# Optimization experiments

Measured on AMD Instinct MI355X. Metric: run time of the kernel, lower is better.

The kernel has to match this reference:

```python
import jax, jax.numpy as jnp
import numpy as np

B, T, C = 4, 2048, 2048
H, S = 32, 64
LN_EPS = 1e-5


def _layer_norm(x, w, b):
    mu = jnp.mean(x, axis=-1, keepdims=True)
    var = jnp.mean((x - mu) ** 2, axis=-1, keepdims=True)
    return (x - mu) / jnp.sqrt(var + LN_EPS) * w + b


def setup_inputs() -> dict:
    key = jax.random.key(0)
    ks = jax.random.split(key, 8)
    sc = 1.0 / np.sqrt(C)
    sc4 = 1.0 / np.sqrt(4 * C)
    return {
        "x": jax.random.normal(ks[0], (B, T, C), jnp.float32),
        "time_decay": jnp.full((H, S), -5.0, jnp.float32),
        "time_first": jnp.zeros((H, S), jnp.float32),
        "Wk": jax.random.normal(ks[1], (C, C), jnp.float32) * sc,
        "Wv": jax.random.normal(ks[2], (C, C), jnp.float32) * sc,
        "Wr": jax.random.normal(ks[3], (C, C), jnp.float32) * sc,
        "Wo": jax.random.normal(ks[4], (C, C), jnp.float32) * sc,
        "Wfk": jax.random.normal(ks[5], (C, 4 * C), jnp.float32) * sc,
        "Wfv": jax.random.normal(ks[6], (4 * C, C), jnp.float32) * sc4,
        "ln1_w": jnp.ones((C,), jnp.float32),
        "ln1_b": jnp.zeros((C,), jnp.float32),
        "ln2_w": jnp.ones((C,), jnp.float32),
        "ln2_b": jnp.zeros((C,), jnp.float32),
    }


def reference(x, time_decay, time_first, Wk, Wv, Wr, Wo, Wfk, Wfv,
              ln1_w, ln1_b, ln2_w, ln2_b):
    b, t, c = x.shape
    h, s = time_decay.shape
    xl = _layer_norm(x, ln1_w, ln1_b)
    k = (xl @ Wk).reshape(b, t, h, s)  # [B,T,H,S]
    v = (xl @ Wv).reshape(b, t, h, s)
    r = (xl @ Wr).reshape(b, t, h, s)

    decay = jnp.exp(-jnp.exp(time_decay))  # [H,S]
    u = jnp.exp(k) * v                      # [B,T,H,S]
    u_t = jnp.swapaxes(u, 0, 1)             # [T,B,H,S]

    def step(state, ut):
        state = decay * state + ut
        return state, state

    _, states = jax.lax.scan(step, jnp.zeros((b, h, s), x.dtype), u_t)  # [T,B,H,S]
    # t=0 bonus term: exp(time_first) * v_0 added to wkv only (not the state)
    states = states.at[0].add(jnp.exp(time_first) * v[:, 0])
    wkv = jnp.swapaxes(states, 0, 1)        # [B,T,H,S]

    rwkv = jax.nn.sigmoid(r) * wkv
    x = x + rwkv.reshape(b, t, c) @ Wo
    xl2 = _layer_norm(x, ln2_w, ln2_b)
    ffn = (jax.nn.relu(xl2 @ Wfk) ** 2) @ Wfv
    return x + ffn
```

## Files before the change

kernel.cpp:

```cpp
#include <hip/hip_runtime.h>
#include <hip/hip_bf16.h>
#include <stdint.h>

#define B_  4
#define T_  2048
#define C_  2048
#define H_  32
#define S_  64
#define M_  (B_ * T_)
#define C4_ (4 * C_)
#define C2_ (2 * C_)
#define LN_EPS 1e-5f
#define NCH 16
#define CLEN 128
#define NCHAN (B_ * C_)

typedef unsigned short u16;
typedef __attribute__((ext_vector_type(8))) short short8;
typedef __attribute__((ext_vector_type(4))) float f32x4;

__device__ __forceinline__ u16 f2bf(float f) {
  uint32_t u = __float_as_uint(f);
  u = (u + 0x7FFFu + ((u >> 16) & 1u)) >> 16;
  return (u16)u;
}
__device__ __forceinline__ float bf2f(u16 u) {
  return __uint_as_float(((uint32_t)u) << 16);
}

__device__ __forceinline__ void gload_lds16(const void* g, void* l) {
  __builtin_amdgcn_global_load_lds(
      (const __attribute__((address_space(1))) uint32_t*)g,
      (__attribute__((address_space(3))) uint32_t*)l, 16, 0, 0);
}

__global__ __launch_bounds__(256) void k_transpose_cast(
    const float* __restrict__ in, u16* __restrict__ out, int ld, int R, int Cn) {
  __shared__ float tile[32][33];
  const int tx = threadIdx.x & 31, ty = threadIdx.x >> 5;
  const int c0 = blockIdx.x * 32, r0 = blockIdx.y * 32;
#pragma unroll
  for (int i = 0; i < 4; ++i) {
    int r = ty + i * 8;
    tile[r][tx] = in[(size_t)(r0 + r) * ld + (c0 + tx)];
  }
  __syncthreads();
#pragma unroll
  for (int i = 0; i < 4; ++i) {
    int cc = ty + i * 8;
    out[(size_t)(c0 + cc) * R + (r0 + tx)] = f2bf(tile[tx][cc]);
  }
}

__global__ __launch_bounds__(256) void k_transpose_cast4(
    const float* __restrict__ w0, const float* __restrict__ w1,
    const float* __restrict__ w2, const float* __restrict__ w3,
    u16* __restrict__ out) {
  __shared__ float tile[32][33];
  const float* in = blockIdx.z == 0 ? w0 : blockIdx.z == 1 ? w1
                  : blockIdx.z == 2 ? w2 : w3;
  u16* o = out + (size_t)blockIdx.z * C_ * C_;
  const int tx = threadIdx.x & 31, ty = threadIdx.x >> 5;
  const int c0 = blockIdx.x * 32, r0 = blockIdx.y * 32;
#pragma unroll
  for (int i = 0; i < 4; ++i) {
    int r = ty + i * 8;
    tile[r][tx] = in[(size_t)(r0 + r) * C_ + (c0 + tx)];
  }
  __syncthreads();
#pragma unroll
  for (int i = 0; i < 4; ++i) {
    int cc = ty + i * 8;
    o[(size_t)(c0 + cc) * C_ + (r0 + tx)] = f2bf(tile[tx][cc]);
  }
}

__global__ __launch_bounds__(256) void k_layernorm_bf16(
    const float* __restrict__ x, const float* __restrict__ w,
    const float* __restrict__ bias, u16* __restrict__ out) {
  const int row = blockIdx.x;
  const int t = threadIdx.x;
  const float* xr = x + (size_t)row * C_;
  float4 a = ((const float4*)xr)[2 * t];
  float4 b = ((const float4*)xr)[2 * t + 1];
  float s = a.x + a.y + a.z + a.w + b.x + b.y + b.z + b.w;
  float q = a.x * a.x + a.y * a.y + a.z * a.z + a.w * a.w +
            b.x * b.x + b.y * b.y + b.z * b.z + b.w * b.w;
#pragma unroll
  for (int off = 32; off > 0; off >>= 1) {
    s += __shfl_down(s, off);
    q += __shfl_down(q, off);
  }
  __shared__ float rs[8];
  const int wv = t >> 6;
  if ((t & 63) == 0) { rs[wv] = s; rs[4 + wv] = q; }
  __syncthreads();
  s = rs[0] + rs[1] + rs[2] + rs[3];
  q = rs[4] + rs[5] + rs[6] + rs[7];
  const float mean = s * (1.0f / C_);
  const float rstd = rsqrtf(q * (1.0f / C_) - mean * mean + LN_EPS);
  float4 w0 = ((const float4*)w)[2 * t], w1 = ((const float4*)w)[2 * t + 1];
  float4 b0 = ((const float4*)bias)[2 * t], b1 = ((const float4*)bias)[2 * t + 1];
  uint4 pk;
  pk.x = (uint32_t)f2bf((a.x - mean) * rstd * w0.x + b0.x) |
         ((uint32_t)f2bf((a.y - mean) * rstd * w0.y + b0.y) << 16);
  pk.y = (uint32_t)f2bf((a.z - mean) * rstd * w0.z + b0.z) |
         ((uint32_t)f2bf((a.w - mean) * rstd * w0.w + b0.w) << 16);
  pk.z = (uint32_t)f2bf((b.x - mean) * rstd * w1.x + b1.x) |
         ((uint32_t)f2bf((b.y - mean) * rstd * w1.y + b1.y) << 16);
  pk.w = (uint32_t)f2bf((b.z - mean) * rstd * w1.z + b1.z) |
         ((uint32_t)f2bf((b.w - mean) * rstd * w1.w + b1.w) << 16);
  ((uint4*)(out + (size_t)row * C_))[t] = pk;
}

__device__ __forceinline__ void stage_half(
    const u16* __restrict__ G, int ldK, int row0, int kcol0,
    u16* lds_half, int tid) {
#pragma unroll
  for (int i = 0; i < 2; ++i) {
    const int slot = i * 512 + tid;
    const int row = slot >> 2;
    const int gs = slot & 3;
    const int gsrc = gs ^ ((row >> 1) & 3);
    gload_lds16(G + (size_t)(row0 + row) * ldK + kcol0 + gsrc * 8,
                ((char*)lds_half) + i * 8192 + (tid >> 6) * 1024);
  }
}

__device__ __forceinline__ short8 frag(const u16* half_base, int row, int g0) {
  const int g = g0 ^ ((row >> 1) & 3);
  return *(const short8*)(half_base + row * 32 + g * 8);
}

template <typename ACC>
__device__ __forceinline__ void gemm_body(
    const u16* __restrict__ A, const u16* __restrict__ Bt,
    int K, int bm0, int bn0, int tid, ACC& acc,
    u16 (*As)[2][256 * 32], u16 (*Bs)[2][256 * 32]) {
  const int wv = tid >> 6, ln = tid & 63;
  const int wm = wv >> 2, wn = wv & 3;
  const int l15 = ln & 15, g0 = ln >> 4;
  const int NT = K >> 6;

  stage_half(A, K, bm0, 0, &As[0][0][0], tid);
  stage_half(Bt, K, bn0, 0, &Bs[0][0][0], tid);
  stage_half(A, K, bm0, 32, &As[0][1][0], tid);
  stage_half(Bt, K, bn0, 32, &Bs[0][1][0], tid);
  asm volatile("s_waitcnt vmcnt(4)" ::: "memory");
  __builtin_amdgcn_s_barrier();
  __builtin_amdgcn_sched_barrier(0);

  for (int t = 0; t < NT; ++t) {
    const int c = t & 1, nb = c ^ 1;
    const int kn = (t + 1) << 6;
    const bool stage_on = (t + 1 < NT);
    const bool lastt = (t + 1 == NT);
    short8 bfr[4], af[4];

#pragma unroll
    for (int h = 0; h < 2; ++h) {
#pragma unroll
      for (int n = 0; n < 4; ++n)
        bfr[n] = frag(&Bs[c][h][0], wn * 64 + n * 16 + l15, g0);
#pragma unroll
      for (int m = 0; m < 4; ++m)
        af[m] = frag(&As[c][h][0], wm * 128 + m * 16 + l15, g0);
      if (stage_on) stage_half(A, K, bm0, kn + h * 32, &As[nb][h][0], tid);
#pragma unroll
      for (int m = 0; m < 4; ++m)
#pragma unroll
        for (int n = 0; n < 4; ++n)
          acc[m][n] = __builtin_amdgcn_mfma_f32_16x16x32_bf16(af[m], bfr[n], acc[m][n], 0, 0, 0);

#pragma unroll
      for (int m = 0; m < 4; ++m)
        af[m] = frag(&As[c][h][0], wm * 128 + 64 + m * 16 + l15, g0);
      if (stage_on) stage_half(Bt, K, bn0, kn + h * 32, &Bs[nb][h][0], tid);
#pragma unroll
      for (int m = 0; m < 4; ++m)
#pragma unroll
        for (int n = 0; n < 4; ++n)
          acc[4 + m][n] = __builtin_amdgcn_mfma_f32_16x16x32_bf16(af[m], bfr[n], acc[4 + m][n], 0, 0, 0);

      if (h == 0) {
        if (!lastt) asm volatile("s_waitcnt vmcnt(4)" ::: "memory");
        else        asm volatile("s_waitcnt vmcnt(0)" ::: "memory");
        __builtin_amdgcn_s_barrier();
        __builtin_amdgcn_sched_barrier(0);
      } else if (!lastt) {
        asm volatile("s_waitcnt vmcnt(4)" ::: "memory");
        __builtin_amdgcn_s_barrier();
        __builtin_amdgcn_sched_barrier(0);
      }
    }
  }
}

template <int EPI>
__global__ __launch_bounds__(512, 2) void k_gemm8(
    const u16* __restrict__ A, const u16* __restrict__ Bt,
    void* __restrict__ Out, const float* __restrict__ Res,
    int M, int N, int K) {
  __shared__ u16 As[2][2][256 * 32];
  __shared__ u16 Bs[2][2][256 * 32];
  const int tid = threadIdx.x;
  const int wv = tid >> 6, ln = tid & 63;
  const int wm = wv >> 2, wn = wv & 3;
  const int l15 = ln & 15;

  const int lin = blockIdx.y * gridDim.x + blockIdx.x;
  const int xcd = lin & 7, slot = lin >> 3;
  const int bx = slot % gridDim.x;
  const int by = xcd * (gridDim.y >> 3) + slot / gridDim.x;
  const int bm0 = by * 256, bn0 = bx * 256;

  f32x4 acc[8][4];
#pragma unroll
  for (int m = 0; m < 8; ++m)
#pragma unroll
    for (int n = 0; n < 4; ++n) acc[m][n] = (f32x4)0.0f;

  gemm_body(A, Bt, K, bm0, bn0, tid, acc, As, Bs);

#pragma unroll
  for (int m = 0; m < 8; ++m) {
    const int r_base = bm0 + wm * 128 + m * 16 + (ln >> 4) * 4;
#pragma unroll
    for (int n = 0; n < 4; ++n) {
      const int cidx = bn0 + wn * 64 + n * 16 + l15;
#pragma unroll
      for (int i = 0; i < 4; ++i) {
        const size_t off = (size_t)(r_base + i) * N + cidx;
        const float v = acc[m][n][i];
        if constexpr (EPI == 0) {
          ((float*)Out)[off] = v;
        } else if constexpr (EPI == 1) {
          ((float*)Out)[off] = Res[off] + v;
        } else if constexpr (EPI == 2) {
          ((u16*)Out)[off] = f2bf(v);
        } else if constexpr (EPI == 3) {
          const float tpos = v > 0.0f ? v : 0.0f;
          ((u16*)Out)[off] = f2bf(tpos * tpos);
        } else {
          ((float*)Out)[off] += v;
        }
      }
    }
  }
}

__global__ __launch_bounds__(512, 2) void k_gemm8_kvr(
    const u16* __restrict__ A, const u16* __restrict__ Wt,
    u16* __restrict__ kb, u16* __restrict__ vb, u16* __restrict__ rb) {
  __shared__ u16 As[2][2][256 * 32];
  __shared__ u16 Bs[2][2][256 * 32];
  const int tid = threadIdx.x;
  const int wv = tid >> 6, ln = tid & 63;
  const int wm = wv >> 2, wn = wv & 3;
  const int l15 = ln & 15;

  const u16* Bt = Wt + (size_t)blockIdx.z * C_ * C_;
  u16* Out = blockIdx.z == 0 ? kb : blockIdx.z == 1 ? vb : rb;

  const int lin = blockIdx.y * gridDim.x + blockIdx.x;
  const int xcd = lin & 7, slot = lin >> 3;
  const int bx = slot % gridDim.x;
  const int by = xcd * (gridDim.y >> 3) + slot / gridDim.x;
  const int bm0 = by * 256, bn0 = bx * 256;

  f32x4 acc[8][4];
#pragma unroll
  for (int m = 0; m < 8; ++m)
#pragma unroll
    for (int n = 0; n < 4; ++n) acc[m][n] = (f32x4)0.0f;

  gemm_body(A, Bt, C_, bm0, bn0, tid, acc, As, Bs);

#pragma unroll
  for (int m = 0; m < 8; ++m) {
    const int r_base = bm0 + wm * 128 + m * 16 + (ln >> 4) * 4;
#pragma unroll
    for (int n = 0; n < 4; ++n) {
      const int cidx = bn0 + wn * 64 + n * 16 + l15;
#pragma unroll
      for (int i = 0; i < 4; ++i)
        Out[(size_t)(r_base + i) * C_ + cidx] = f2bf(acc[m][n][i]);
    }
  }
}

__global__ __launch_bounds__(256) void k_scan_a(
    const u16* __restrict__ kk, const u16* __restrict__ vv,
    const float* __restrict__ td, float* __restrict__ Sloc) {
  const int g = blockIdx.x * 256 + threadIdx.x;
  const int j = blockIdx.y;
  const int ch = g & (C_ - 1);
  const float d = __expf(-__expf(td[ch]));
  const size_t base = ((size_t)(g >> 11) * T_ + (size_t)j * CLEN) * C_ + ch;
  float s = 0.0f;
#pragma unroll 4
  for (int t = 0; t < CLEN; ++t) {
    const size_t idx = base + (size_t)t * C_;
    s = d * s + __expf(bf2f(kk[idx])) * bf2f(vv[idx]);
  }
  Sloc[(size_t)j * NCHAN + g] = s;
}

__global__ __launch_bounds__(256) void k_scan_b(
    const float* __restrict__ td, const float* __restrict__ Sloc,
    float* __restrict__ carry) {
  const int g = blockIdx.x * 256 + threadIdx.x;
  const int ch = g & (C_ - 1);
  const float dL = __expf(-__expf(td[ch]) * (float)CLEN);
  float s = 0.0f;
#pragma unroll
  for (int j = 0; j < NCH; ++j) {
    carry[(size_t)j * NCHAN + g] = s;
    s = dL * s + Sloc[(size_t)j * NCHAN + g];
  }
}

__global__ __launch_bounds__(256) void k_scan_c(
    const u16* __restrict__ kk, const u16* __restrict__ vv,
    const u16* __restrict__ rr, const float* __restrict__ td,
    const float* __restrict__ tf, const float* __restrict__ carry,
    u16* __restrict__ rwkv) {
  const int g = blockIdx.x * 256 + threadIdx.x;
  const int j = blockIdx.y;
  const int ch = g & (C_ - 1);
  const float d = __expf(-__expf(td[ch]));
  const float bonus = __expf(tf[ch]);
  const size_t base = ((size_t)(g >> 11) * T_ + (size_t)j * CLEN) * C_ + ch;
  float s = carry[(size_t)j * NCHAN + g];
#pragma unroll 2
  for (int t = 0; t < CLEN; ++t) {
    const size_t idx = base + (size_t)t * C_;
    const float vval = bf2f(vv[idx]);
    s = d * s + __expf(bf2f(kk[idx])) * vval;
    float wkv = s;
    if (j == 0 && t == 0) wkv += bonus * vval;
    const float rv = bf2f(rr[idx]);
    const float sg = 1.0f / (1.0f + __expf(-rv));
    rwkv[idx] = f2bf(sg * wkv);
  }
}

extern "C" void kernel_launch(void* const* d_in, const int* in_sizes, int n_in,
                              void* d_out, int out_size, void* d_ws, size_t ws_size,
                              hipStream_t stream) {
  const float* x    = (const float*)d_in[0];
  const float* td   = (const float*)d_in[1];
  const float* tf   = (const float*)d_in[2];
  const float* Wk   = (const float*)d_in[3];
  const float* Wv   = (const float*)d_in[4];
  const float* Wr   = (const float*)d_in[5];
  const float* Wo   = (const float*)d_in[6];
  const float* Wfk  = (const float*)d_in[7];
  const float* Wfv  = (const float*)d_in[8];
  const float* ln1w = (const float*)d_in[9];
  const float* ln1b = (const float*)d_in[10];
  const float* ln2w = (const float*)d_in[11];
  const float* ln2b = (const float*)d_in[12];
  float* out = (float*)d_out;

  char* p = (char*)d_ws;
  auto alloc = [&](size_t bytes) {
    char* r = p;
    p += (bytes + 255) & ~(size_t)255;
    return r;
  };
  u16*   wbuf = (u16*)alloc((size_t)4 * C_ * C_ * 2);
  u16*   xl   = (u16*)alloc((size_t)M_ * C_ * 2);
  u16*   kbuf = (u16*)alloc((size_t)M_ * C_ * 2);
  u16*   vbuf = (u16*)alloc((size_t)M_ * C_ * 2);
  u16*   rbuf = (u16*)alloc((size_t)M_ * C_ * 2);
  float* Sloc = (float*)alloc((size_t)NCH * NCHAN * 4);
  float* carry = (float*)alloc((size_t)NCH * NCHAN * 4);
  u16* rwkv = rbuf;
  u16* hchunk = xl;
  u16* wfbuf = rbuf;

  const dim3 ggrid(C_ / 256, M_ / 256);

  k_layernorm_bf16<<<M_, 256, 0, stream>>>(x, ln1w, ln1b, xl);

  k_transpose_cast4<<<dim3(C_ / 32, C_ / 32, 4), 256, 0, stream>>>(
      Wk, Wv, Wr, Wo, wbuf);

  k_gemm8_kvr<<<dim3(C_ / 256, M_ / 256, 3), 512, 0, stream>>>(
      xl, wbuf, kbuf, vbuf, rbuf);

  k_scan_a<<<dim3(NCHAN / 256, NCH), 256, 0, stream>>>(kbuf, vbuf, td, Sloc);
  k_scan_b<<<dim3(NCHAN / 256), 256, 0, stream>>>(td, Sloc, carry);
  k_scan_c<<<dim3(NCHAN / 256, NCH), 256, 0, stream>>>(kbuf, vbuf, rbuf, td, tf, carry, rwkv);

  k_gemm8<1><<<ggrid, 512, 0, stream>>>(rwkv, wbuf + (size_t)3 * C_ * C_, out, x, M_, C_, C_);

  u16* xl2 = vbuf;
  k_layernorm_bf16<<<M_, 256, 0, stream>>>(out, ln2w, ln2b, xl2);

  for (int c = 0; c < 2; ++c) {
    k_transpose_cast<<<dim3(C2_ / 32, C_ / 32), 256, 0, stream>>>(
        Wfk + (size_t)c * C2_, wfbuf, C4_, C_, C2_);
    k_gemm8<3><<<dim3(C2_ / 256, M_ / 256), 512, 0, stream>>>(
        xl2, wfbuf, hchunk, nullptr, M_, C2_, C_);
    k_transpose_cast<<<dim3(C_ / 32, C2_ / 32), 256, 0, stream>>>(
        Wfv + (size_t)c * C2_ * C_, wfbuf, C_, C2_, C_);
    k_gemm8<4><<<dim3(C_ / 256, M_ / 256), 512, 0, stream>>>(
        hchunk, wfbuf, out, nullptr, M_, C_, C2_);
  }
}
```

Baseline: 968.8 us.

## Batch FFN weight casts and up-projection into single wide launches when workspace allows

When the workspace is large enough, the FFN is restructured. All four C×C slices of Wfk and Wfv are transposed and cast in one z-batched launch each. The whole 4C up-projection with squared-ReLU runs as one 4-slab grid into four separate bf16 buffers. The down-projection then runs as two GEMMs, each reading its K range from two buffers through a new split-K staging path. This removes per-chunk launch serialization and gives larger grids, at the cost of an extra activation buffer and a workspace-size-dependent code path.

```diff
diff --git a/kernel.cpp b/kernel.cpp
--- a/kernel.cpp
+++ b/kernel.cpp
@@ -37,6 +37,27 @@
 __global__ __launch_bounds__(256) void k_transpose_cast(
     const float* __restrict__ in, u16* __restrict__ out, int ld, int R, int Cn) {
   __shared__ float tile[32][33];
+  const int tx = threadIdx.x & 31, ty = threadIdx.x >> 5;
+  const int c0 = blockIdx.x * 32, r0 = blockIdx.y * 32;
+#pragma unroll
+  for (int i = 0; i < 4; ++i) {
+    int r = ty + i * 8;
+    tile[r][tx] = in[(size_t)(r0 + r) * ld + (c0 + tx)];
+  }
+  __syncthreads();
+#pragma unroll
+  for (int i = 0; i < 4; ++i) {
+    int cc = ty + i * 8;
+    out[(size_t)(c0 + cc) * R + (r0 + tx)] = f2bf(tile[tx][cc]);
+  }
+}
+
+__global__ __launch_bounds__(256) void k_transpose_castZ(
+    const float* __restrict__ in0, size_t in_zoff,
+    u16* __restrict__ out0, size_t out_zoff, int ld, int R, int Cn) {
+  __shared__ float tile[32][33];
+  const float* in = in0 + in_zoff * blockIdx.z;
+  u16* out = out0 + out_zoff * blockIdx.z;
   const int tx = threadIdx.x & 31, ty = threadIdx.x >> 5;
   const int c0 = blockIdx.x * 32, r0 = blockIdx.y * 32;
 #pragma unroll
@@ -132,20 +153,39 @@
   return *(const short8*)(half_base + row * 32 + g * 8);
 }
 
-template <typename ACC>
+template <bool SPLIT, typename ACC>
 __device__ __forceinline__ void gemm_body(
-    const u16* __restrict__ A, const u16* __restrict__ Bt,
+    const u16* __restrict__ A1, const u16* __restrict__ A2,
+    const u16* __restrict__ B1, const u16* __restrict__ B2,
     int K, int bm0, int bn0, int tid, ACC& acc,
     u16 (*As)[2][256 * 32], u16 (*Bs)[2][256 * 32]) {
   const int wv = tid >> 6, ln = tid & 63;
   const int wm = wv >> 2, wn = wv & 3;
   const int l15 = ln & 15, g0 = ln >> 4;
   const int NT = K >> 6;
-
-  stage_half(A, K, bm0, 0, &As[0][0][0], tid);
-  stage_half(Bt, K, bn0, 0, &Bs[0][0][0], tid);
-  stage_half(A, K, bm0, 32, &As[0][1][0], tid);
-  stage_half(Bt, K, bn0, 32, &Bs[0][1][0], tid);
+  const int Ksp = K >> 1;
+
+  auto stageA = [&](int kcol, u16* dst) {
+    if constexpr (SPLIT) {
+      if (kcol < Ksp) stage_half(A1, Ksp, bm0, kcol, dst, tid);
+      else            stage_half(A2, Ksp, bm0, kcol - Ksp, dst, tid);
+    } else {
+      stage_half(A1, K, bm0, kcol, dst, tid);
+    }
+  };
+  auto stageB = [&](int kcol, u16* dst) {
+    if constexpr (SPLIT) {
+      if (kcol < Ksp) stage_half(B1, Ksp, bn0, kcol, dst, tid);
+      else            stage_half(B2, Ksp, bn0, kcol - Ksp, dst, tid);
+    } else {
+      stage_half(B1, K, bn0, kcol, dst, tid);
+    }
+  };
+
+  stageA(0, &As[0][0][0]);
+  stageB(0, &Bs[0][0][0]);
+  stageA(32, &As[0][1][0]);
+  stageB(32, &Bs[0][1][0]);
   asm volatile("s_waitcnt vmcnt(4)" ::: "memory");
   __builtin_amdgcn_s_barrier();
   __builtin_amdgcn_sched_barrier(0);
@@ -165,7 +205,7 @@
 #pragma unroll
       for (int m = 0; m < 4; ++m)
         af[m] = frag(&As[c][h][0], wm * 128 + m * 16 + l15, g0);
-      if (stage_on) stage_half(A, K, bm0, kn + h * 32, &As[nb][h][0], tid);
+      if (stage_on) stageA(kn + h * 32, &As[nb][h][0]);
 #pragma unroll
       for (int m = 0; m < 4; ++m)
 #pragma unroll
@@ -175,7 +215,7 @@
 #pragma unroll
       for (int m = 0; m < 4; ++m)
         af[m] = frag(&As[c][h][0], wm * 128 + 64 + m * 16 + l15, g0);
-      if (stage_on) stage_half(Bt, K, bn0, kn + h * 32, &Bs[nb][h][0], tid);
+      if (stage_on) stageB(kn + h * 32, &Bs[nb][h][0]);
 #pragma unroll
       for (int m = 0; m < 4; ++m)
 #pragma unroll
@@ -196,9 +236,18 @@
   }
 }
 
-template <int EPI>
+__device__ __forceinline__ void xcd_remap(int& bm0, int& bn0) {
+  const int lin = blockIdx.y * gridDim.x + blockIdx.x;
+  const int xcd = lin & 7, slot = lin >> 3;
+  const int bx = slot % gridDim.x;
+  const int by = xcd * (gridDim.y >> 3) + slot / gridDim.x;
+  bm0 = by * 256; bn0 = bx * 256;
+}
+
+template <int EPI, bool SPLIT>
 __global__ __launch_bounds__(512, 2) void k_gemm8(
-    const u16* __restrict__ A, const u16* __restrict__ Bt,
+    const u16* __restrict__ A1, const u16* __restrict__ A2,
+    const u16* __restrict__ B1, const u16* __restrict__ B2,
     void* __restrict__ Out, const float* __restrict__ Res,
     int M, int N, int K) {
   __shared__ u16 As[2][2][256 * 32];
@@ -207,12 +256,8 @@
   const int wv = tid >> 6, ln = tid & 63;
   const int wm = wv >> 2, wn = wv & 3;
   const int l15 = ln & 15;
-
-  const int lin = blockIdx.y * gridDim.x + blockIdx.x;
-  const int xcd = lin & 7, slot = lin >> 3;
-  const int bx = slot % gridDim.x;
-  const int by = xcd * (gridDim.y >> 3) + slot / gridDim.x;
-  const int bm0 = by * 256, bn0 = bx * 256;
+  int bm0, bn0;
+  xcd_remap(bm0, bn0);
 
   f32x4 acc[8][4];
 #pragma unroll
@@ -220,7 +265,7 @@
 #pragma unroll
     for (int n = 0; n < 4; ++n) acc[m][n] = (f32x4)0.0f;
 
-  gemm_body(A, Bt, K, bm0, bn0, tid, acc, As, Bs);
+  gemm_body<SPLIT>(A1, A2, B1, B2, K, bm0, bn0, tid, acc, As, Bs);
 
 #pragma unroll
   for (int m = 0; m < 8; ++m) {
@@ -258,15 +303,10 @@
   const int wv = tid >> 6, ln = tid & 63;
   const int wm = wv >> 2, wn = wv & 3;
   const int l15 = ln & 15;
-
   const u16* Bt = Wt + (size_t)blockIdx.z * C_ * C_;
   u16* Out = blockIdx.z == 0 ? kb : blockIdx.z == 1 ? vb : rb;
-
-  const int lin = blockIdx.y * gridDim.x + blockIdx.x;
-  const int xcd = lin & 7, slot = lin >> 3;
-  const int bx = slot % gridDim.x;
-  const int by = xcd * (gridDim.y >> 3) + slot / gridDim.x;
-  const int bm0 = by * 256, bn0 = bx * 256;
+  int bm0, bn0;
+  xcd_remap(bm0, bn0);
 
   f32x4 acc[8][4];
 #pragma unroll
@@ -274,7 +314,7 @@
 #pragma unroll
     for (int n = 0; n < 4; ++n) acc[m][n] = (f32x4)0.0f;
 
-  gemm_body(A, Bt, C_, bm0, bn0, tid, acc, As, Bs);
+  gemm_body<false>(A, nullptr, Bt, nullptr, C_, bm0, bn0, tid, acc, As, Bs);
 
 #pragma unroll
   for (int m = 0; m < 8; ++m) {
@@ -285,6 +325,46 @@
 #pragma unroll
       for (int i = 0; i < 4; ++i)
         Out[(size_t)(r_base + i) * C_ + cidx] = f2bf(acc[m][n][i]);
+    }
+  }
+}
+
+__global__ __launch_bounds__(512, 2) void k_gemm8_ffk4(
+    const u16* __restrict__ A, const u16* __restrict__ Wt,
+    u16* __restrict__ o0, u16* __restrict__ o1,
+    u16* __restrict__ o2, u16* __restrict__ o3) {
+  __shared__ u16 As[2][2][256 * 32];
+  __shared__ u16 Bs[2][2][256 * 32];
+  const int tid = threadIdx.x;
+  const int wv = tid >> 6, ln = tid & 63;
+  const int wm = wv >> 2, wn = wv & 3;
+  const int l15 = ln & 15;
+  const u16* Bt = Wt + (size_t)blockIdx.z * C_ * C_;
+  u16* Out = blockIdx.z == 0 ? o0 : blockIdx.z == 1 ? o1
+           : blockIdx.z == 2 ? o2 : o3;
+  int bm0, bn0;
+  xcd_remap(bm0, bn0);
+
+  f32x4 acc[8][4];
+#pragma unroll
+  for (int m = 0; m < 8; ++m)
+#pragma unroll
+    for (int n = 0; n < 4; ++n) acc[m][n] = (f32x4)0.0f;
+
+  gemm_body<false>(A, nullptr, Bt, nullptr, C_, bm0, bn0, tid, acc, As, Bs);
+
+#pragma unroll
+  for (int m = 0; m < 8; ++m) {
+    const int r_base = bm0 + wm * 128 + m * 16 + (ln >> 4) * 4;
+#pragma unroll
+    for (int n = 0; n < 4; ++n) {
+      const int cidx = bn0 + wn * 64 + n * 16 + l15;
+#pragma unroll
+      for (int i = 0; i < 4; ++i) {
+        const float v = acc[m][n][i];
+        const float tpos = v > 0.0f ? v : 0.0f;
+        Out[(size_t)(r_base + i) * C_ + cidx] = f2bf(tpos * tpos);
+      }
     }
   }
 }
@@ -363,6 +443,8 @@
   const float* ln2b = (const float*)d_in[12];
   float* out = (float*)d_out;
 
+  const bool big = ws_size >= (size_t)203000000;
+
   char* p = (char*)d_ws;
   auto alloc = [&](size_t bytes) {
     char* r = p;
@@ -374,6 +456,7 @@
   u16*   kbuf = (u16*)alloc((size_t)M_ * C_ * 2);
   u16*   vbuf = (u16*)alloc((size_t)M_ * C_ * 2);
   u16*   rbuf = (u16*)alloc((size_t)M_ * C_ * 2);
+  u16*   h3   = big ? (u16*)alloc((size_t)M_ * C_ * 2) : nullptr;
   float* Sloc = (float*)alloc((size_t)NCH * NCHAN * 4);
   float* carry = (float*)alloc((size_t)NCH * NCHAN * 4);
   u16* rwkv = rbuf;
@@ -394,19 +477,34 @@
   k_scan_b<<<dim3(NCHAN / 256), 256, 0, stream>>>(td, Sloc, carry);
   k_scan_c<<<dim3(NCHAN / 256, NCH), 256, 0, stream>>>(kbuf, vbuf, rbuf, td, tf, carry, rwkv);
 
-  k_gemm8<1><<<ggrid, 512, 0, stream>>>(rwkv, wbuf + (size_t)3 * C_ * C_, out, x, M_, C_, C_);
+  k_gemm8<1, false><<<ggrid, 512, 0, stream>>>(
+      rwkv, nullptr, wbuf + (size_t)3 * C_ * C_, nullptr, out, x, M_, C_, C_);
 
   u16* xl2 = vbuf;
   k_layernorm_bf16<<<M_, 256, 0, stream>>>(out, ln2w, ln2b, xl2);
 
-  for (int c = 0; c < 2; ++c) {
-    k_transpose_cast<<<dim3(C2_ / 32, C_ / 32), 256, 0, stream>>>(
-        Wfk + (size_t)c * C2_, wfbuf, C4_, C_, C2_);
-    k_gemm8<3><<<dim3(C2_ / 256, M_ / 256), 512, 0, stream>>>(
-        xl2, wfbuf, hchunk, nullptr, M_, C2_, C_);
-    k_transpose_cast<<<dim3(C_ / 32, C2_ / 32), 256, 0, stream>>>(
-        Wfv + (size_t)c * C2_ * C_, wfbuf, C_, C2_, C_);
-    k_gemm8<4><<<dim3(C_ / 256, M_ / 256), 512, 0, stream>>>(
-        hchunk, wfbuf, out, nullptr, M_, C_, C2_);
-  }
-}
+  if (big) {
+    k_transpose_castZ<<<dim3(C_ / 32, C_ / 32, 4), 256, 0, stream>>>(
+        Wfk, (size_t)C_, wbuf, (size_t)C_ * C_, C4_, C_, C_);
+    k_gemm8_ffk4<<<dim3(C_ / 256, M_ / 256, 4), 512, 0, stream>>>(
+        xl2, wbuf, xl, kbuf, rbuf, h3);
+    k_transpose_castZ<<<dim3(C_ / 32, C_ / 32, 4), 256, 0, stream>>>(
+        Wfv, (size_t)C_ * C_, wbuf, (size_t)C_ * C_, C_, C_, C_);
+    k_gemm8<4, true><<<ggrid, 512, 0, stream>>>(
+        xl, kbuf, wbuf, wbuf + (size_t)C_ * C_, out, nullptr, M_, C_, C2_);
+    k_gemm8<4, true><<<ggrid, 512, 0, stream>>>(
+        rbuf, h3, wbuf + (size_t)2 * C_ * C_, wbuf + (size_t)3 * C_ * C_,
+        out, nullptr, M_, C_, C2_);
+  } else {
+    for (int c = 0; c < 2; ++c) {
+      k_transpose_cast<<<dim3(C2_ / 32, C_ / 32), 256, 0, stream>>>(
+          Wfk + (size_t)c * C2_, wfbuf, C4_, C_, C2_);
+      k_gemm8<3, false><<<dim3(C2_ / 256, M_ / 256), 512, 0, stream>>>(
+          xl2, nullptr, wfbuf, nullptr, hchunk, nullptr, M_, C2_, C_);
+      k_transpose_cast<<<dim3(C_ / 32, C2_ / 32), 256, 0, stream>>>(
+          Wfv + (size_t)c * C2_ * C_, wfbuf, C_, C2_, C_);
+      k_gemm8<4, false><<<dim3(C_ / 256, M_ / 256), 512, 0, stream>>>(
+          hchunk, nullptr, wfbuf, nullptr, out, nullptr, M_, C_, C2_);
+    }
+  }
+}
```

New measurement: 988.7 us. +2.0%, slower.
